# Kernel optimization log

Measured on AMD Instinct MI355X. Metric: run time of the kernel, lower is better.

The kernel has to match this reference:

```python
import jax, jax.numpy as jnp
import numpy as np

B, NN, K, F = 256, 90, 10, 90  # graphs, nodes/graph, retain_node, node_len
TENDENCY = 0.7


def setup_inputs() -> dict:
    key = jax.random.key(0)
    ks = jax.random.split(key, 16)
    N = B * NN
    # fully-connected (no self-loop) edge list per graph, block-offset per graph
    a = np.repeat(np.arange(NN), NN)
    b = np.tile(np.arange(NN), NN)
    m = a != b
    src0, dst0 = a[m], b[m]                      # [8010]
    off = (np.arange(B) * NN)[:, None]
    src = (src0[None, :] + off).ravel()
    dst = (dst0[None, :] + off).ravel()
    edge_index = jnp.asarray(np.stack([src, dst]), dtype=jnp.int64)
    E = edge_index.shape[1]
    batch = jnp.asarray(np.repeat(np.arange(B), NN), dtype=jnp.int64)
    s = 1.0 / np.sqrt(F)
    return {
        "x": jax.random.normal(ks[0], (N, F), jnp.float32),
        "edge_index": edge_index,
        "edge_attr": jax.random.uniform(ks[1], (E,), jnp.float32),
        "batch": batch,
        "W1r": jax.random.normal(ks[2], (F, F), jnp.float32) * s,
        "W1m": jax.random.normal(ks[3], (F, F), jnp.float32) * s,
        "b1": jnp.zeros((F,), jnp.float32),
        "W2r": jax.random.normal(ks[4], (F, F), jnp.float32) * s,
        "W2m": jax.random.normal(ks[5], (F, F), jnp.float32) * s,
        "b2": jnp.zeros((F,), jnp.float32),
        "pool_p": jax.random.normal(ks[6], (F,), jnp.float32),
        "lin_W": jax.random.normal(ks[7], (K * F, 2 * K * F + 1), jnp.float32) / np.sqrt(K * F),
        "lin_b": jnp.zeros((2 * K * F + 1,), jnp.float32),
        "cls_W": jax.random.normal(ks[8], (2 * K * F + 1, 1), jnp.float32) / np.sqrt(2 * K * F + 1),
        "cls_b": jnp.zeros((1,), jnp.float32),
    }


def reference(x, edge_index, edge_attr, batch, W1r, W1m, b1, W2r, W2m, b2,
              pool_p, lin_W, lin_b, cls_W, cls_b):
    src, dst = edge_index[0], edge_index[1]
    N = x.shape[0]

    def conv(h, Wr, Wm, b):  # edge-conditioned message passing
        msg = (h[src] @ Wm) * edge_attr[:, None]          # [E, F]
        agg = jax.ops.segment_sum(msg, dst, num_segments=N)
        return jax.nn.relu(h @ Wr + agg + b)

    def bn(h):  # fresh BatchNorm1d (gamma=1, beta=0), training-mode batch stats
        mu = h.mean(axis=0)
        var = h.var(axis=0)
        return (h - mu) * jax.lax.rsqrt(var + 1e-5)

    x = bn(conv(x, W1r, W1m, b1))
    x = bn(conv(x, W2r, W2m, b2))

    # category-aware top-k pooling: projection score, keep K nodes per graph
    score = TENDENCY * jnp.tanh((x @ pool_p) / jnp.linalg.norm(pool_p))  # [N]
    vals, idx = jax.lax.top_k(score.reshape(B, NN), K)                   # [B, K]
    xb = x.reshape(B, NN, F)
    xs = jnp.take_along_axis(xb, idx[:, :, None], axis=1) * vals[:, :, None]
    perm = (idx + (jnp.arange(B) * NN)[:, None]).reshape(-1)             # global node ids

    h = xs.reshape(B, K * F)
    h = h @ lin_W + lin_b
    out = jax.nn.sigmoid((h @ cls_W + cls_b).reshape(-1))                # [B]
    return (out, perm)
```

## Files before the change

kernel.cpp:

```cpp
#include <hip/hip_runtime.h>
#include <math.h>

#define NG   90
#define PD   96
#define STRD 100
#define KK   10
#define NB   256
#define NTOT (NB*NG)
#define EPG  8010
#define ARR  (PD*STRD)
#define SM_FLOATS (4*ARR + 4*96)

__global__ __launch_bounds__(256, 1)
void layer_kernel(const float* __restrict__ xin, const float* __restrict__ gsIn, int apply_bn,
                  const float* __restrict__ attr,
                  const float* __restrict__ Wm, const float* __restrict__ Wr,
                  const float* __restrict__ bias,
                  float* __restrict__ hout, float* __restrict__ gsOut,
                  int do_prep,
                  const float* __restrict__ linW, const float* __restrict__ linb,
                  const float* __restrict__ clsW, const float* __restrict__ clsb,
                  const float* __restrict__ poolp,
                  float* __restrict__ vlin, float* __restrict__ scal)
{
    extern __shared__ float sm[];
    float* sXM = sm;
    float* sA  = sXM + ARR;
    float* sWm = sA + ARR;
    float* sWr = sWm + ARR;
    float* sSum = sWr + ARR;
    float* sSq  = sSum + 96;
    float* sMu  = sSq + 96;
    float* sRs  = sMu + 96;

    const int g = blockIdx.x, tid = threadIdx.x;
    const int lane = tid & 63, wave = tid >> 6;
    const int lr = lane >> 3, lc = lane & 7;
    const int r0 = (wave >> 1) * 48 + lr * 6;
    const int c0 = (wave & 1) * 48 + lc * 6;

    if (tid < 96) {
        sSum[tid] = 0.f; sSq[tid] = 0.f;
        float m = 0.f, r = 1.f;
        if (apply_bn && tid < NG) {
            m = gsIn[tid] * (1.f / NTOT);
            float v = gsIn[96 + tid] * (1.f / NTOT) - m * m;
            r = rsqrtf(v + 1e-5f);
        }
        sMu[tid] = m; sRs[tid] = r;
    }
    __syncthreads();

    for (int idx = tid; idx < PD * PD; idx += 256) {
        int r = idx / PD, k = idx - (idx / PD) * PD;
        float v = 0.f;
        if (r < NG && k < NG) v = (xin[(size_t)(g * NG + r) * NG + k] - sMu[k]) * sRs[k];
        sXM[r * STRD + k] = v;
    }
    for (int idx = tid; idx < PD * PD; idx += 256) {
        int d = idx / PD, s = idx - (idx / PD) * PD;
        float v = 0.f;
        if (d < NG && s < NG && s != d) v = attr[(size_t)g * EPG + s * 89 + (d > s ? d - 1 : d)];
        sA[d * STRD + s] = v;
    }
    for (int idx = tid; idx < PD * PD; idx += 256) {
        int c = idx / PD, k = idx - (idx / PD) * PD;
        float vm = 0.f, vr = 0.f;
        if (c < NG && k < NG) { vm = Wm[k * NG + c]; vr = Wr[k * NG + c]; }
        sWm[c * STRD + k] = vm;
        sWr[c * STRD + k] = vr;
    }
    float bj[6];
#pragma unroll
    for (int j = 0; j < 6; j++) bj[j] = (c0 + j < NG) ? bias[c0 + j] : 0.f;
    __syncthreads();

    float accM[6][6], accR[6][6];
#pragma unroll
    for (int i = 0; i < 6; i++)
#pragma unroll
        for (int j = 0; j < 6; j++) { accM[i][j] = 0.f; accR[i][j] = 0.f; }
    {
        const float* pX  = sXM + r0 * STRD;
        const float* pWm = sWm + c0 * STRD;
        const float* pWr = sWr + c0 * STRD;
#pragma unroll 2
        for (int k = 0; k < PD; k += 4) {
            float4 xv[6], wm[6], wr[6];
#pragma unroll
            for (int i = 0; i < 6; i++) xv[i] = *(const float4*)(pX + i * STRD + k);
#pragma unroll
            for (int j = 0; j < 6; j++) {
                wm[j] = *(const float4*)(pWm + j * STRD + k);
                wr[j] = *(const float4*)(pWr + j * STRD + k);
            }
#pragma unroll
            for (int i = 0; i < 6; i++)
#pragma unroll
                for (int j = 0; j < 6; j++) {
                    accM[i][j] = fmaf(xv[i].x, wm[j].x, accM[i][j]);
                    accM[i][j] = fmaf(xv[i].y, wm[j].y, accM[i][j]);
                    accM[i][j] = fmaf(xv[i].z, wm[j].z, accM[i][j]);
                    accM[i][j] = fmaf(xv[i].w, wm[j].w, accM[i][j]);
                    accR[i][j] = fmaf(xv[i].x, wr[j].x, accR[i][j]);
                    accR[i][j] = fmaf(xv[i].y, wr[j].y, accR[i][j]);
                    accR[i][j] = fmaf(xv[i].z, wr[j].z, accR[i][j]);
                    accR[i][j] = fmaf(xv[i].w, wr[j].w, accR[i][j]);
                }
        }
    }
    __syncthreads();

#pragma unroll
    for (int j = 0; j < 6; j++)
#pragma unroll
        for (int i = 0; i < 6; i++)
            sXM[(c0 + j) * STRD + (r0 + i)] = accM[i][j];
    __syncthreads();

    float h[6][6];
#pragma unroll
    for (int i = 0; i < 6; i++)
#pragma unroll
        for (int j = 0; j < 6; j++) h[i][j] = accR[i][j] + bj[j];
    {
        const float* pA = sA  + r0 * STRD;
        const float* pM = sXM + c0 * STRD;
#pragma unroll 2
        for (int k = 0; k < PD; k += 4) {
            float4 av[6], mv[6];
#pragma unroll
            for (int i = 0; i < 6; i++) av[i] = *(const float4*)(pA + i * STRD + k);
#pragma unroll
            for (int j = 0; j < 6; j++) mv[j] = *(const float4*)(pM + j * STRD + k);
#pragma unroll
            for (int i = 0; i < 6; i++)
#pragma unroll
                for (int j = 0; j < 6; j++) {
                    h[i][j] = fmaf(av[i].x, mv[j].x, h[i][j]);
                    h[i][j] = fmaf(av[i].y, mv[j].y, h[i][j]);
                    h[i][j] = fmaf(av[i].z, mv[j].z, h[i][j]);
                    h[i][j] = fmaf(av[i].w, mv[j].w, h[i][j]);
                }
        }
    }

    float cs[6], cq[6];
#pragma unroll
    for (int j = 0; j < 6; j++) { cs[j] = 0.f; cq[j] = 0.f; }
#pragma unroll
    for (int i = 0; i < 6; i++) {
        int r = r0 + i;
        if (r < NG) {
#pragma unroll
            for (int j = 0; j < 6; j++) {
                int c = c0 + j;
                if (c < NG) {
                    float v = fmaxf(h[i][j], 0.f);
                    hout[(size_t)(g * NG + r) * NG + c] = v;
                    cs[j] += v; cq[j] += v * v;
                }
            }
        }
    }
#pragma unroll
    for (int m = 8; m < 64; m <<= 1) {
#pragma unroll
        for (int j = 0; j < 6; j++) {
            cs[j] += __shfl_xor(cs[j], m);
            cq[j] += __shfl_xor(cq[j], m);
        }
    }
    if (lr == 0) {
#pragma unroll
        for (int j = 0; j < 6; j++) {
            int c = c0 + j;
            if (c < NG) { atomicAdd(&sSum[c], cs[j]); atomicAdd(&sSq[c], cq[j]); }
        }
    }
    __syncthreads();
    if (tid < NG) { atomicAdd(&gsOut[tid], sSum[tid]); atomicAdd(&gsOut[96 + tid], sSq[tid]); }

    if (do_prep) {
        if (g < 225) {
            int j = g * 4 + wave;
            const float* row = linW + (size_t)j * 1801;
            float acc = 0.f;
            for (int c = lane; c < 1801; c += 64) acc += row[c] * clsW[c];
            for (int off = 32; off; off >>= 1) acc += __shfl_down(acc, off);
            if (lane == 0) vlin[j] = acc;
        } else if (g == 255) {
            if (wave == 0) {
                float acc = 0.f;
                for (int c = lane; c < 1801; c += 64) acc += linb[c] * clsW[c];
                for (int off = 32; off; off >>= 1) acc += __shfl_down(acc, off);
                if (lane == 0) scal[0] = acc + clsb[0];
            } else if (wave == 1) {
                float acc = 0.f;
                for (int c = lane; c < NG; c += 64) acc += poolp[c] * poolp[c];
                for (int off = 32; off; off >>= 1) acc += __shfl_down(acc, off);
                if (lane == 0) scal[1] = rsqrtf(acc);
            }
        }
    }
}

__global__ __launch_bounds__(256)
void final_kernel(const float* __restrict__ h2,
                  const float* __restrict__ gsum, const float* __restrict__ gsq,
                  const float* __restrict__ poolp,
                  const float* __restrict__ vlin, const float* __restrict__ scal,
                  float* __restrict__ out)
{
    __shared__ float sXN[NG * 91];
    __shared__ float sMu[96], sRs[96], sP[96];
    __shared__ float sScore[NG];
    __shared__ int   sIdx[KK];
    __shared__ float sVal[KK];
    __shared__ float sRed[4];
    const int g = blockIdx.x, tid = threadIdx.x;

    if (tid < NG) {
        float m = gsum[tid] * (1.f / NTOT);
        float v = gsq[tid] * (1.f / NTOT) - m * m;
        sMu[tid] = m; sRs[tid] = rsqrtf(v + 1e-5f);
        sP[tid] = poolp[tid];
    }
    __syncthreads();

    const float* hg = h2 + (size_t)g * (NG * NG);
    for (int idx = tid; idx < NG * NG; idx += 256) {
        int d = idx / NG, f = idx - (idx / NG) * NG;
        sXN[d * 91 + f] = (hg[idx] - sMu[f]) * sRs[f];
    }
    __syncthreads();

    if (tid < NG) {
        float s = 0.f;
        for (int f = 0; f < NG; f++) s += sXN[tid * 91 + f] * sP[f];
        sScore[tid] = 0.7f * tanhf(s * scal[1]);
    }
    __syncthreads();

    if (tid < 64) {
        float va = sScore[tid];
        float vb = (tid + 64 < NG) ? sScore[tid + 64] : -1e30f;
        int ia = tid, ib = tid + 64;
        for (int k = 0; k < KK; k++) {
            float v; int i;
            if (va >= vb) { v = va; i = ia; } else { v = vb; i = ib; }
            for (int off = 1; off < 64; off <<= 1) {
                float v2 = __shfl_xor(v, off);
                int   i2 = __shfl_xor(i, off);
                if (v2 > v || (v2 == v && i2 < i)) { v = v2; i = i2; }
            }
            if (tid == 0) { sIdx[k] = i; sVal[k] = v; }
            if (i == ia) va = -1e30f;
            if (i == ib) vb = -1e30f;
        }
    }
    __syncthreads();

    if (tid < KK) out[NB + g * KK + tid] = (float)(g * NG + sIdx[tid]);

    float acc = 0.f;
    for (int j = tid; j < KK * NG; j += 256) {
        int k = j / NG, f = j - (j / NG) * NG;
        acc += sXN[sIdx[k] * 91 + f] * sVal[k] * vlin[j];
    }
    for (int off = 32; off; off >>= 1) acc += __shfl_down(acc, off);
    if ((tid & 63) == 0) sRed[tid >> 6] = acc;
    __syncthreads();
    if (tid == 0) {
        float tot = sRed[0] + sRed[1] + sRed[2] + sRed[3] + scal[0];
        out[g] = 1.f / (1.f + expf(-tot));
    }
}

extern "C" void kernel_launch(void* const* d_in, const int* in_sizes, int n_in,
                              void* d_out, int out_size, void* d_ws, size_t ws_size,
                              hipStream_t stream) {
    const float* x    = (const float*)d_in[0];
    const float* attr = (const float*)d_in[2];
    const float* W1r  = (const float*)d_in[4];
    const float* W1m  = (const float*)d_in[5];
    const float* b1   = (const float*)d_in[6];
    const float* W2r  = (const float*)d_in[7];
    const float* W2m  = (const float*)d_in[8];
    const float* b2   = (const float*)d_in[9];
    const float* poolp= (const float*)d_in[10];
    const float* linW = (const float*)d_in[11];
    const float* linb = (const float*)d_in[12];
    const float* clsW = (const float*)d_in[13];
    const float* clsb = (const float*)d_in[14];

    float* ws     = (float*)d_ws;
    float* gstats = ws;
    float* vlin   = ws + 384;
    float* scal   = ws + 1284;
    float* h1     = ws + 2048;
    float* h2     = h1 + (size_t)NTOT * NG;

    hipMemsetAsync(gstats, 0, 384 * sizeof(float), stream);

    const size_t smem = SM_FLOATS * sizeof(float);
    hipFuncSetAttribute((const void*)layer_kernel, hipFuncAttributeMaxDynamicSharedMemorySize, (int)smem);

    layer_kernel<<<NB, 256, smem, stream>>>(x,  gstats, 0, attr, W1m, W1r, b1, h1, gstats,
                                            1, linW, linb, clsW, clsb, poolp, vlin, scal);
    layer_kernel<<<NB, 256, smem, stream>>>(h1, gstats, 1, attr, W2m, W2r, b2, h2, gstats + 192,
                                            0, linW, linb, clsW, clsb, poolp, vlin, scal);

    final_kernel<<<NB, 256, 0, stream>>>(h2, gstats + 192, gstats + 288, poolp, vlin, scal, (float*)d_out);
}
```

Measured before the change: 241.7 us.

## Use 512-thread blocks with interleaved column tiles and per-block BN partial stats

Layer kernel now runs 512 threads per block, and each thread computes a 3x6 tile whose columns are strided by 16 instead of a contiguous 6x6 tile. This is meant to expose more parallelism per graph and to change the LDS access pattern. Global atomics on the BatchNorm statistics are replaced by per-block partial sums that the next kernel reduces, which also removes the memset. The linear-head precompute is spread across all blocks. The cost is a redundant 256-way reduction of the partial stats in every consumer block.

```diff
diff --git a/kernel.cpp b/kernel.cpp
--- a/kernel.cpp
+++ b/kernel.cpp
@@ -9,14 +9,15 @@
 #define NTOT (NB*NG)
 #define EPG  8010
 #define ARR  (PD*STRD)
-#define SM_FLOATS (4*ARR + 4*96)
-
-__global__ __launch_bounds__(256, 1)
-void layer_kernel(const float* __restrict__ xin, const float* __restrict__ gsIn, int apply_bn,
+#define SM_FLOATS (4*ARR)
+
+__global__ __launch_bounds__(512, 2)
+void layer_kernel(const float* __restrict__ xin,
+                  const float* __restrict__ psIn, int apply_bn,
                   const float* __restrict__ attr,
                   const float* __restrict__ Wm, const float* __restrict__ Wr,
                   const float* __restrict__ bias,
-                  float* __restrict__ hout, float* __restrict__ gsOut,
+                  float* __restrict__ hout, float* __restrict__ psOut,
                   int do_prep,
                   const float* __restrict__ linW, const float* __restrict__ linb,
                   const float* __restrict__ clsW, const float* __restrict__ clsb,
@@ -24,78 +25,76 @@
                   float* __restrict__ vlin, float* __restrict__ scal)
 {
     extern __shared__ float sm[];
-    float* sXM = sm;
-    float* sA  = sXM + ARR;
+    float* s0  = sm;
+    float* sA  = s0 + ARR;
     float* sWm = sA + ARR;
     float* sWr = sWm + ARR;
-    float* sSum = sWr + ARR;
-    float* sSq  = sSum + 96;
-    float* sMu  = sSq + 96;
-    float* sRs  = sMu + 96;
+    __shared__ float sSum[96], sSq[96], sMu[96], sRs[96], sStat[192];
 
     const int g = blockIdx.x, tid = threadIdx.x;
     const int lane = tid & 63, wave = tid >> 6;
-    const int lr = lane >> 3, lc = lane & 7;
-    const int r0 = (wave >> 1) * 48 + lr * 6;
-    const int c0 = (wave & 1) * 48 + lc * 6;
-
-    if (tid < 96) {
-        sSum[tid] = 0.f; sSq[tid] = 0.f;
-        float m = 0.f, r = 1.f;
-        if (apply_bn && tid < NG) {
-            m = gsIn[tid] * (1.f / NTOT);
-            float v = gsIn[96 + tid] * (1.f / NTOT) - m * m;
-            r = rsqrtf(v + 1e-5f);
-        }
-        sMu[tid] = m; sRs[tid] = r;
-    }
-    __syncthreads();
-
-    for (int idx = tid; idx < PD * PD; idx += 256) {
+    const int cg = tid & 15;
+    const int rg = tid >> 4;
+    const int r0 = rg * 3;
+
+    if (apply_bn) {
+        if (tid < 192) {
+            float s = 0.f;
+            const float* p = psIn + tid;
+#pragma unroll 8
+            for (int b = 0; b < NB; b++) s += p[b * 192];
+            sStat[tid] = s;
+        }
+        __syncthreads();
+        if (tid < 96) {
+            float m = sStat[tid] * (1.f / NTOT);
+            float v = sStat[96 + tid] * (1.f / NTOT) - m * m;
+            sMu[tid] = m; sRs[tid] = rsqrtf(v + 1e-5f);
+        }
+    } else if (tid < 96) { sMu[tid] = 0.f; sRs[tid] = 1.f; }
+    if (tid < 96) { sSum[tid] = 0.f; sSq[tid] = 0.f; }
+    __syncthreads();
+
+    for (int idx = tid; idx < PD * PD; idx += 512) {
         int r = idx / PD, k = idx - (idx / PD) * PD;
         float v = 0.f;
         if (r < NG && k < NG) v = (xin[(size_t)(g * NG + r) * NG + k] - sMu[k]) * sRs[k];
-        sXM[r * STRD + k] = v;
-    }
-    for (int idx = tid; idx < PD * PD; idx += 256) {
-        int d = idx / PD, s = idx - (idx / PD) * PD;
+        s0[r * STRD + k] = v;
+    }
+    for (int idx = tid; idx < PD * PD; idx += 512) {
+        int s = idx / PD, d = idx - (idx / PD) * PD;
         float v = 0.f;
-        if (d < NG && s < NG && s != d) v = attr[(size_t)g * EPG + s * 89 + (d > s ? d - 1 : d)];
+        if (s < NG && d < NG && d != s) v = attr[(size_t)g * EPG + s * 89 + (d > s ? d - 1 : d)];
         sA[d * STRD + s] = v;
     }
-    for (int idx = tid; idx < PD * PD; idx += 256) {
-        int c = idx / PD, k = idx - (idx / PD) * PD;
-        float vm = 0.f, vr = 0.f;
-        if (c < NG && k < NG) { vm = Wm[k * NG + c]; vr = Wr[k * NG + c]; }
-        sWm[c * STRD + k] = vm;
-        sWr[c * STRD + k] = vr;
-    }
-    float bj[6];
-#pragma unroll
-    for (int j = 0; j < 6; j++) bj[j] = (c0 + j < NG) ? bias[c0 + j] : 0.f;
-    __syncthreads();
-
-    float accM[6][6], accR[6][6];
-#pragma unroll
-    for (int i = 0; i < 6; i++)
+    for (int idx = tid; idx < PD * PD; idx += 512) {
+        int k = idx / PD, c = idx - (idx / PD) * PD;
+        bool ok = (k < NG && c < NG);
+        sWm[c * STRD + k] = ok ? Wm[k * NG + c] : 0.f;
+        sWr[c * STRD + k] = ok ? Wr[k * NG + c] : 0.f;
+    }
+    __syncthreads();
+
+    float accM[3][6], accR[3][6];
+#pragma unroll
+    for (int i = 0; i < 3; i++)
 #pragma unroll
         for (int j = 0; j < 6; j++) { accM[i][j] = 0.f; accR[i][j] = 0.f; }
     {
-        const float* pX  = sXM + r0 * STRD;
-        const float* pWm = sWm + c0 * STRD;
-        const float* pWr = sWr + c0 * STRD;
+        const float* pX = s0 + r0 * STRD;
 #pragma unroll 2
         for (int k = 0; k < PD; k += 4) {
-            float4 xv[6], wm[6], wr[6];
-#pragma unroll
-            for (int i = 0; i < 6; i++) xv[i] = *(const float4*)(pX + i * STRD + k);
+            float4 xv[3], wm[6], wr[6];
+#pragma unroll
+            for (int i = 0; i < 3; i++) xv[i] = *(const float4*)(pX + i * STRD + k);
 #pragma unroll
             for (int j = 0; j < 6; j++) {
-                wm[j] = *(const float4*)(pWm + j * STRD + k);
-                wr[j] = *(const float4*)(pWr + j * STRD + k);
+                const int c = cg + 16 * j;
+                wm[j] = *(const float4*)(sWm + c * STRD + k);
+                wr[j] = *(const float4*)(sWr + c * STRD + k);
             }
 #pragma unroll
-            for (int i = 0; i < 6; i++)
+            for (int i = 0; i < 3; i++)
 #pragma unroll
                 for (int j = 0; j < 6; j++) {
                     accM[i][j] = fmaf(xv[i].x, wm[j].x, accM[i][j]);
@@ -114,27 +113,29 @@
 #pragma unroll
     for (int j = 0; j < 6; j++)
 #pragma unroll
-        for (int i = 0; i < 6; i++)
-            sXM[(c0 + j) * STRD + (r0 + i)] = accM[i][j];
-    __syncthreads();
-
-    float h[6][6];
-#pragma unroll
-    for (int i = 0; i < 6; i++)
-#pragma unroll
-        for (int j = 0; j < 6; j++) h[i][j] = accR[i][j] + bj[j];
+        for (int i = 0; i < 3; i++)
+            s0[(cg + 16 * j) * STRD + (r0 + i)] = accM[i][j];
+    __syncthreads();
+
+    float h[3][6];
+#pragma unroll
+    for (int j = 0; j < 6; j++) {
+        const int c = cg + 16 * j;
+        float bj = (c < NG) ? bias[c] : 0.f;
+#pragma unroll
+        for (int i = 0; i < 3; i++) h[i][j] = accR[i][j] + bj;
+    }
     {
-        const float* pA = sA  + r0 * STRD;
-        const float* pM = sXM + c0 * STRD;
+        const float* pA = sA + r0 * STRD;
 #pragma unroll 2
         for (int k = 0; k < PD; k += 4) {
-            float4 av[6], mv[6];
-#pragma unroll
-            for (int i = 0; i < 6; i++) av[i] = *(const float4*)(pA + i * STRD + k);
-#pragma unroll
-            for (int j = 0; j < 6; j++) mv[j] = *(const float4*)(pM + j * STRD + k);
-#pragma unroll
-            for (int i = 0; i < 6; i++)
+            float4 av[3], mv[6];
+#pragma unroll
+            for (int i = 0; i < 3; i++) av[i] = *(const float4*)(pA + i * STRD + k);
+#pragma unroll
+            for (int j = 0; j < 6; j++) mv[j] = *(const float4*)(s0 + (cg + 16 * j) * STRD + k);
+#pragma unroll
+            for (int i = 0; i < 3; i++)
 #pragma unroll
                 for (int j = 0; j < 6; j++) {
                     h[i][j] = fmaf(av[i].x, mv[j].x, h[i][j]);
@@ -149,12 +150,12 @@
 #pragma unroll
     for (int j = 0; j < 6; j++) { cs[j] = 0.f; cq[j] = 0.f; }
 #pragma unroll
-    for (int i = 0; i < 6; i++) {
+    for (int i = 0; i < 3; i++) {
         int r = r0 + i;
         if (r < NG) {
 #pragma unroll
             for (int j = 0; j < 6; j++) {
-                int c = c0 + j;
+                int c = cg + 16 * j;
                 if (c < NG) {
                     float v = fmaxf(h[i][j], 0.f);
                     hout[(size_t)(g * NG + r) * NG + c] = v;
@@ -164,65 +165,73 @@
         }
     }
 #pragma unroll
-    for (int m = 8; m < 64; m <<= 1) {
+    for (int m = 16; m < 64; m <<= 1) {
 #pragma unroll
         for (int j = 0; j < 6; j++) {
             cs[j] += __shfl_xor(cs[j], m);
             cq[j] += __shfl_xor(cq[j], m);
         }
     }
-    if (lr == 0) {
+    if ((lane >> 4) == 0) {
 #pragma unroll
         for (int j = 0; j < 6; j++) {
-            int c = c0 + j;
+            int c = cg + 16 * j;
             if (c < NG) { atomicAdd(&sSum[c], cs[j]); atomicAdd(&sSq[c], cq[j]); }
         }
     }
     __syncthreads();
-    if (tid < NG) { atomicAdd(&gsOut[tid], sSum[tid]); atomicAdd(&gsOut[96 + tid], sSq[tid]); }
+    if (tid < 96) psOut[g * 192 + tid] = sSum[tid];
+    else if (tid < 192) psOut[g * 192 + tid] = sSq[tid - 96];
 
     if (do_prep) {
-        if (g < 225) {
-            int j = g * 4 + wave;
-            const float* row = linW + (size_t)j * 1801;
+        if (wave < 4) {
+            int row = g + 256 * wave;
+            if (row < 900) {
+                const float* rw = linW + (size_t)row * 1801;
+                float acc = 0.f;
+                for (int c2 = lane; c2 < 1801; c2 += 64) acc += rw[c2] * clsW[c2];
+                for (int off = 32; off; off >>= 1) acc += __shfl_down(acc, off);
+                if (lane == 0) vlin[row] = acc;
+            }
+        } else if (g == 0 && wave == 4) {
             float acc = 0.f;
-            for (int c = lane; c < 1801; c += 64) acc += row[c] * clsW[c];
+            for (int c2 = lane; c2 < 1801; c2 += 64) acc += linb[c2] * clsW[c2];
             for (int off = 32; off; off >>= 1) acc += __shfl_down(acc, off);
-            if (lane == 0) vlin[j] = acc;
-        } else if (g == 255) {
-            if (wave == 0) {
-                float acc = 0.f;
-                for (int c = lane; c < 1801; c += 64) acc += linb[c] * clsW[c];
-                for (int off = 32; off; off >>= 1) acc += __shfl_down(acc, off);
-                if (lane == 0) scal[0] = acc + clsb[0];
-            } else if (wave == 1) {
-                float acc = 0.f;
-                for (int c = lane; c < NG; c += 64) acc += poolp[c] * poolp[c];
-                for (int off = 32; off; off >>= 1) acc += __shfl_down(acc, off);
-                if (lane == 0) scal[1] = rsqrtf(acc);
-            }
+            if (lane == 0) scal[0] = acc + clsb[0];
+        } else if (g == 0 && wave == 5) {
+            float acc = 0.f;
+            for (int c2 = lane; c2 < NG; c2 += 64) acc += poolp[c2] * poolp[c2];
+            for (int off = 32; off; off >>= 1) acc += __shfl_down(acc, off);
+            if (lane == 0) scal[1] = rsqrtf(acc);
         }
     }
 }
 
 __global__ __launch_bounds__(256)
-void final_kernel(const float* __restrict__ h2,
-                  const float* __restrict__ gsum, const float* __restrict__ gsq,
+void final_kernel(const float* __restrict__ h2, const float* __restrict__ psIn,
                   const float* __restrict__ poolp,
                   const float* __restrict__ vlin, const float* __restrict__ scal,
                   float* __restrict__ out)
 {
     __shared__ float sXN[NG * 91];
-    __shared__ float sMu[96], sRs[96], sP[96];
+    __shared__ float sMu[96], sRs[96], sP[96], sStat[192];
     __shared__ float sScore[NG];
     __shared__ int   sIdx[KK];
     __shared__ float sVal[KK];
     __shared__ float sRed[4];
     const int g = blockIdx.x, tid = threadIdx.x;
 
+    if (tid < 192) {
+        float s = 0.f;
+        const float* p = psIn + tid;
+#pragma unroll 8
+        for (int b = 0; b < NB; b++) s += p[b * 192];
+        sStat[tid] = s;
+    }
+    __syncthreads();
     if (tid < NG) {
-        float m = gsum[tid] * (1.f / NTOT);
-        float v = gsq[tid] * (1.f / NTOT) - m * m;
+        float m = sStat[tid] * (1.f / NTOT);
+        float v = sStat[96 + tid] * (1.f / NTOT) - m * m;
         sMu[tid] = m; sRs[tid] = rsqrtf(v + 1e-5f);
         sP[tid] = poolp[tid];
     }
@@ -294,22 +303,20 @@
     const float* clsW = (const float*)d_in[13];
     const float* clsb = (const float*)d_in[14];
 
-    float* ws     = (float*)d_ws;
-    float* gstats = ws;
-    float* vlin   = ws + 384;
-    float* scal   = ws + 1284;
-    float* h1     = ws + 2048;
-    float* h2     = h1 + (size_t)NTOT * NG;
-
-    hipMemsetAsync(gstats, 0, 384 * sizeof(float), stream);
+    float* ws   = (float*)d_ws;
+    float* ps1  = ws;
+    float* ps2  = ps1 + NB * 192;
+    float* vlin = ps2 + NB * 192;
+    float* scal = vlin + 900;
+    float* h1   = scal + 62;
+    float* h2   = h1 + (size_t)NTOT * NG;
 
     const size_t smem = SM_FLOATS * sizeof(float);
     hipFuncSetAttribute((const void*)layer_kernel, hipFuncAttributeMaxDynamicSharedMemorySize, (int)smem);
 
-    layer_kernel<<<NB, 256, smem, stream>>>(x,  gstats, 0, attr, W1m, W1r, b1, h1, gstats,
+    layer_kernel<<<NB, 512, smem, stream>>>(x,  nullptr, 0, attr, W1m, W1r, b1, h1, ps1,
                                             1, linW, linb, clsW, clsb, poolp, vlin, scal);
-    layer_kernel<<<NB, 256, smem, stream>>>(h1, gstats, 1, attr, W2m, W2r, b2, h2, gstats + 192,
+    layer_kernel<<<NB, 512, smem, stream>>>(h1, ps1, 1, attr, W2m, W2r, b2, h2, ps2,
                                             0, linW, linb, clsW, clsb, poolp, vlin, scal);
-
-    final_kernel<<<NB, 256, 0, stream>>>(h2, gstats + 192, gstats + 288, poolp, vlin, scal, (float*)d_out);
+    final_kernel<<<NB, 256, 0, stream>>>(h2, ps2, poolp, vlin, scal, (float*)d_out);
 }
```

Result: faster. 234.4 us (-3.1%).
